# Optimization experiments

Hardware: AMD Instinct MI355X
Metric: run time of the kernel (lower is better)

Reference implementation:

```python
import jax, jax.numpy as jnp
import numpy as np

B, S = 2048, 4096
RANK = 8            # bilinear rank and gain projector rank
LOW_GAIN = 1.0
LOW_SIGMA = 0.2
HIGH_GAIN = 0.5
HIGH_CUTOFF = 0.6


def setup_inputs() -> dict:
    key = jax.random.key(0)
    ks = jax.random.split(key, 12)
    sc = 0.05
    inp = {
        "x": jax.random.normal(ks[0], (B, S), dtype=jnp.float32),
        # ComplexLinear U, V: (rank, state_size) real+imag weights
        "Ur": jax.random.normal(ks[1], (RANK, S), dtype=jnp.float32) * sc,
        "Ui": jax.random.normal(ks[2], (RANK, S), dtype=jnp.float32) * sc,
        "Vr": jax.random.normal(ks[3], (RANK, S), dtype=jnp.float32) * sc,
        "Vi": jax.random.normal(ks[4], (RANK, S), dtype=jnp.float32) * sc,
        # ComplexLinear W: (state_size, rank) -- zero-init in source; random here to exercise math
        "Wr": jax.random.normal(ks[5], (S, RANK), dtype=jnp.float32) * sc,
        "Wi": jax.random.normal(ks[6], (S, RANK), dtype=jnp.float32) * sc,
        # dynamic spectral gain MLP: Linear(2S, r) -> ReLU -> Linear(r, S)
        "P1w": jax.random.normal(ks[7], (RANK, 2 * S), dtype=jnp.float32) * 0.01,
        "P1b": jnp.zeros((RANK,), dtype=jnp.float32),
        "P2w": jax.random.normal(ks[8], (S, RANK), dtype=jnp.float32) * 0.01,
        "P2b": jax.random.normal(ks[9], (S,), dtype=jnp.float32) * 0.01,
        "alpha": jnp.ones((), dtype=jnp.float32),
    }
    return inp


def _complex_linear(z, wr, wi):
    # y = z @ (wr + i*wi)^T for complex z, real weights of shape (out, in)
    w = (wr + 1j * wi).astype(jnp.complex64)
    return z @ w.T


def _fixed_spectral_gain(nf):
    low_boost = LOW_GAIN * jnp.exp(-0.5 * jnp.square(nf / LOW_SIGMA))
    tw = max(0.05, 0.25 * max(0.05, 1.0 - HIGH_CUTOFF))
    high_damp = HIGH_GAIN * jax.nn.sigmoid((nf - HIGH_CUTOFF) / tw)
    return jnp.maximum(1.0 + low_boost - high_damp, 0.0)


def reference(x, Ur, Ui, Vr, Vi, Wr, Wi, P1w, P1b, P2w, P2b, alpha):
    s = x.shape[-1]
    z = jnp.fft.fft(x, axis=-1).astype(jnp.complex64)  # [B, S] complex spectrum

    # normalized frequency in [0, 1]
    nf = (jnp.abs(jnp.fft.fftfreq(s)) * 2.0).astype(jnp.float32)  # [S]
    base_gain = _fixed_spectral_gain(nf)                          # [S]

    # dynamic spectral delta: small MLP on concatenated real/imag spectrum features
    feat = jnp.concatenate([z.real, z.imag], axis=-1)             # [B, 2S]
    hidden = jax.nn.relu(feat @ P1w.T + P1b)                      # [B, r]
    delta = hidden @ P2w.T + P2b                                  # [B, S]

    # radial (isotropic) interpolation of delta onto the frequency grid
    pos = jnp.clip(nf, 0.0, 1.0)
    scaled = pos * (s - 1)
    lower = jnp.floor(scaled).astype(jnp.int32)
    upper = jnp.ceil(scaled).astype(jnp.int32)
    frac = (scaled - lower.astype(jnp.float32))[None, :]          # [1, S]
    d_lo = delta[:, lower]                                        # [B, S]
    d_hi = delta[:, upper]
    delta_i = d_lo + (d_hi - d_lo) * frac

    gain = jnp.maximum(base_gain[None, :] + alpha * delta_i, 0.0)  # [B, S]
    z = z * gain.astype(jnp.complex64)

    # cross-dimensional complex bilinear coupling (low rank)
    p = _complex_linear(z, Ur, Ui)          # [B, r]
    q = _complex_linear(z, Vr, Vi)          # [B, r]
    gamma = p * jnp.conj(q)                 # [B, r]
    z = z + _complex_linear(gamma, Wr, Wi)  # [B, S]

    return jnp.fft.ifft(z, axis=-1).real.astype(jnp.float32)
```

## Files before the change

### kernel.cpp

```cpp
#include <hip/hip_runtime.h>

#define S_LEN 4096
#define NT 512
#define PER 8
#define RANK 8
#define BP 4160
#define NHALF 2049
#define TWO_PI 6.2831853071795864769f

__device__ __forceinline__ void cmul(float& xr, float& xi, float cr, float ci){
    float tr = xr*cr - xi*ci;
    xi = xr*ci + xi*cr;
    xr = tr;
}

template<int SIGN>
__device__ __forceinline__ void dft4(float& ar,float& ai,float& br,float& bi,
                                     float& cr,float& ci,float& dr,float& di){
    float Ar=ar+cr, Ai=ai+ci;
    float Br=ar-cr, Bi=ai-ci;
    float Cr=br+dr, Ci=bi+di;
    float Dr, Di;
    if (SIGN < 0){ Dr = bi-di; Di = dr-br; }
    else         { Dr = di-bi; Di = br-dr; }
    ar=Ar+Cr; ai=Ai+Ci;
    br=Br+Dr; bi=Bi+Di;
    cr=Ar-Cr; ci=Ai-Ci;
    dr=Br-Dr; di=Bi-Di;
}

template<int SIGN>
__device__ __forceinline__ void dft8(float ur[8], float ui[8]){
    const float h = 0.70710678118654752f;
    float er0=ur[0], ei0=ui[0], er1=ur[2], ei1=ui[2];
    float er2=ur[4], ei2=ui[4], er3=ur[6], ei3=ui[6];
    float fr0=ur[1], fi0=ui[1], fr1=ur[3], fi1=ui[3];
    float fr2=ur[5], fi2=ui[5], fr3=ur[7], fi3=ui[7];
    dft4<SIGN>(er0,ei0, er1,ei1, er2,ei2, er3,ei3);
    dft4<SIGN>(fr0,fi0, fr1,fi1, fr2,fi2, fr3,fi3);
    {   const float c =  h, s_ = (SIGN<0) ? -h : h;
        cmul(fr1, fi1, c, s_); }
    {   float tr = fr2, ti = fi2;
        if (SIGN < 0){ fr2 =  ti; fi2 = -tr; }
        else         { fr2 = -ti; fi2 =  tr; }
    }
    {   const float c = -h, s_ = (SIGN<0) ? -h : h;
        cmul(fr3, fi3, c, s_); }
    ur[0]=er0+fr0; ui[0]=ei0+fi0;
    ur[1]=er1+fr1; ui[1]=ei1+fi1;
    ur[2]=er2+fr2; ui[2]=ei2+fi2;
    ur[3]=er3+fr3; ui[3]=ei3+fi3;
    ur[4]=er0-fr0; ui[4]=ei0-fi0;
    ur[5]=er1-fr1; ui[5]=ei1-fi1;
    ur[6]=er2-fr2; ui[6]=ei2-fi2;
    ur[7]=er3-fr3; ui[7]=ei3-fi3;
}

template<int SIGN>
__device__ __forceinline__ void twiddle8(float ur[8], float ui[8], float theta){
    float s, c;
    __sincosf(theta, &s, &c);
    const float wi = (SIGN < 0) ? -s : s;
    const float wr = c;
    float pr = wr, pi = wi;
    cmul(ur[1], ui[1], pr, pi);
#pragma unroll
    for (int m=2;m<8;m++){
        float nr = pr*wr - pi*wi;
        pi = pr*wi + pi*wr;
        pr = nr;
        cmul(ur[m], ui[m], pr, pi);
    }
}

__device__ __forceinline__ void gain_pair(int k, const float* hhA, const float* hhB,
    float alpha, const float* __restrict__ P2w, const float* __restrict__ P2b,
    float& ga, float& gb){
    float nf = (float)k * (1.0f/2048.0f);
    float tt = nf * 5.0f;
    float lb = __expf(-0.5f * tt * tt);
    float hd = 0.5f / (1.0f + __expf(-(nf - 0.6f) * 10.0f));
    float bg = fmaxf(1.0f + lb - hd, 0.0f);
    float scaled = nf * 4095.0f;
    float fl = floorf(scaled);
    int lo = (int)fl;
    int hi = (int)ceilf(scaled);
    float fr = scaled - fl;
    const float4* p2lo = (const float4*)(P2w + (size_t)lo * RANK);
    const float4* p2hi = (const float4*)(P2w + (size_t)hi * RANK);
    float4 a0 = p2lo[0], a1 = p2lo[1];
    float4 b0 = p2hi[0], b1 = p2hi[1];
    float blo = P2b[lo], bhi = P2b[hi];
    float dAlo = blo + hhA[0]*a0.x + hhA[1]*a0.y + hhA[2]*a0.z + hhA[3]*a0.w
                     + hhA[4]*a1.x + hhA[5]*a1.y + hhA[6]*a1.z + hhA[7]*a1.w;
    float dAhi = bhi + hhA[0]*b0.x + hhA[1]*b0.y + hhA[2]*b0.z + hhA[3]*b0.w
                     + hhA[4]*b1.x + hhA[5]*b1.y + hhA[6]*b1.z + hhA[7]*b1.w;
    float dBlo = blo + hhB[0]*a0.x + hhB[1]*a0.y + hhB[2]*a0.z + hhB[3]*a0.w
                     + hhB[4]*a1.x + hhB[5]*a1.y + hhB[6]*a1.z + hhB[7]*a1.w;
    float dBhi = bhi + hhB[0]*b0.x + hhB[1]*b0.y + hhB[2]*b0.z + hhB[3]*b0.w
                     + hhB[4]*b1.x + hhB[5]*b1.y + hhB[6]*b1.z + hhB[7]*b1.w;
    float dA = dAlo + (dAhi - dAlo) * fr;
    float dB = dBlo + (dBhi - dBlo) * fr;
    ga = fmaxf(bg + alpha * dA, 0.0f);
    gb = fmaxf(bg + alpha * dB, 0.0f);
}


__global__ __launch_bounds__(NT, 4) void recip_mixer(
    const float* __restrict__ x,
    const float* __restrict__ Ur, const float* __restrict__ Ui,
    const float* __restrict__ Vr, const float* __restrict__ Vi,
    const float* __restrict__ Wr, const float* __restrict__ Wi,
    const float* __restrict__ P1w, const float* __restrict__ P1b,
    const float* __restrict__ P2w, const float* __restrict__ P2b,
    const float* __restrict__ alphap,
    float* __restrict__ out)
{
    __shared__ float sre[BP], sim[BP];
    __shared__ float gA[NHALF], gB[NHALF];
    __shared__ float red[256];
    __shared__ float hidA[RANK], hidB[RANK];
    __shared__ float4 gam4[RANK];
    __shared__ float pqs[64];

    const int t    = threadIdx.x;
    const int pairidx = blockIdx.x;
    const int lane = t & 63;
    const int wid  = t >> 6;

    float ur[8], ui[8];

    const int baseA = (t & 63) + 512 * (t >> 6);
    const int baseB = (t & 7) + 8*(t >> 6) + 520*((t >> 3) & 7);
    const int baseC = (t >> 3) + 520*(t & 7);

    const float* xa = x + (size_t)(2 * pairidx) * S_LEN;
    const float* xb = xa + S_LEN;

    {
#pragma unroll
        for (int c=0;c<8;c++){ ur[c] = xa[t + 512*c]; ui[c] = xb[t + 512*c]; }
        dft8<-1>(ur, ui);
#pragma unroll
        for (int e=0;e<8;e++){ sre[baseA + 64*e] = ur[e]; sim[baseA + 64*e] = ui[e]; }
    }
    __syncthreads();
    {
#pragma unroll
        for (int m=0;m<8;m++){ ur[m] = sre[t + 512*m]; ui[m] = sim[t + 512*m]; }
        twiddle8<-1>(ur, ui, TWO_PI * (float)(t >> 6) * (1.0f/64.0f));
        dft8<-1>(ur, ui);
        __syncthreads();
#pragma unroll
        for (int e=0;e<8;e++){ sre[baseB + 64*e] = ur[e]; sim[baseB + 64*e] = ui[e]; }
    }
    __syncthreads();
    {
#pragma unroll
        for (int m=0;m<8;m++){ ur[m] = sre[t + 520*m]; ui[m] = sim[t + 520*m]; }
        twiddle8<-1>(ur, ui, TWO_PI * (float)(t >> 3) * (1.0f/512.0f));
        dft8<-1>(ur, ui);
        __syncthreads();
#pragma unroll
        for (int e=0;e<8;e++){ sre[baseC + 64*e] = ur[e]; sim[baseC + 64*e] = ui[e]; }
    }
    __syncthreads();
    {
#pragma unroll
        for (int m=0;m<8;m++){ ur[m] = sre[t + 520*m]; ui[m] = sim[t + 520*m]; }
        twiddle8<-1>(ur, ui, TWO_PI * (float)t * (1.0f/4096.0f));
        dft8<-1>(ur, ui);
        __syncthreads();
#pragma unroll
        for (int e=0;e<8;e++){ sre[t + 512*e] = ur[e]; sim[t + 512*e] = ui[e]; }
    }
    __syncthreads();

    {
        float ha[RANK], hb[RANK];
#pragma unroll
        for (int r = 0; r < RANK; r++){ ha[r] = 0.0f; hb[r] = 0.0f; }
#pragma unroll 1
        for (int i = 0; i < PER; i++) {
            int k = t + NT * i;
            int j = (S_LEN - k) & (S_LEN - 1);
            float ar = sre[k], ai = sim[k];
            float br = sre[j], bi = sim[j];
            float zar = 0.5f*(ar + br), zai = 0.5f*(ai - bi);
            float zbr = 0.5f*(ai + bi), zbi = 0.5f*(br - ar);
#pragma unroll
            for (int r = 0; r < RANK; r++) {
                float p0 = P1w[r * (2 * S_LEN) + k];
                float p1 = P1w[r * (2 * S_LEN) + S_LEN + k];
                ha[r] += zar * p0 + zai * p1;
                hb[r] += zbr * p0 + zbi * p1;
            }
        }
#pragma unroll
        for (int r = 0; r < RANK; r++) {
#pragma unroll
            for (int off = 32; off > 0; off >>= 1){
                ha[r] += __shfl_xor(ha[r], off, 64);
                hb[r] += __shfl_xor(hb[r], off, 64);
            }
        }
        if (lane == 0) {
#pragma unroll
            for (int r = 0; r < RANK; r++){
                red[wid * 16 + r]     = ha[r];
                red[wid * 16 + 8 + r] = hb[r];
            }
        }
        __syncthreads();
        if (t < 16) {
            float v = 0.0f;
#pragma unroll
            for (int w = 0; w < 8; w++) v += red[w * 16 + t];
            float res = fmaxf(v + P1b[t & 7], 0.0f);
            if (t < 8) hidA[t] = res; else hidB[t - 8] = res;
        }
        __syncthreads();
    }

    {
        float hhA[RANK], hhB[RANK];
#pragma unroll
        for (int r = 0; r < RANK; r++){ hhA[r] = hidA[r]; hhB[r] = hidB[r]; }
        const float alpha = alphap[0];
#pragma unroll 1
        for (int i = 0; i < 4; i++) {
            int k = t + 512 * i;
            float ga, gb;
            gain_pair(k, hhA, hhB, alpha, P2w, P2b, ga, gb);
            gA[k] = ga; gB[k] = gb;
        }
        if (t == 0) {
            float ga, gb;
            gain_pair(2048, hhA, hhB, alpha, P2w, P2b, ga, gb);
            gA[2048] = ga; gB[2048] = gb;
        }
    }
    __syncthreads();

    {
        float pAr[RANK], pAi[RANK], pBr[RANK], pBi[RANK];
#pragma unroll
        for (int r = 0; r < RANK; r++){ pAr[r]=0.f; pAi[r]=0.f; pBr[r]=0.f; pBi[r]=0.f; }
#pragma unroll 1
        for (int i = 0; i < PER; i++) {
            int k = t + NT * i;
            int j = (S_LEN - k) & (S_LEN - 1);
            int m = (k <= 2048) ? k : (S_LEN - k);
            float ar = sre[k], ai = sim[k];
            float br = sre[j], bi = sim[j];
            float ga = gA[m], gb = gB[m];
            float zar = 0.5f*ga*(ar + br), zai = 0.5f*ga*(ai - bi);
            float zbr = 0.5f*gb*(ai + bi), zbi = 0.5f*gb*(br - ar);
#pragma unroll
            for (int r = 0; r < RANK; r++) {
                float u_ = Ur[r * S_LEN + k], v_ = Ui[r * S_LEN + k];
                pAr[r] += zar * u_ - zai * v_;
                pAi[r] += zar * v_ + zai * u_;
                pBr[r] += zbr * u_ - zbi * v_;
                pBi[r] += zbr * v_ + zbi * u_;
            }
        }
#pragma unroll
        for (int r = 0; r < RANK; r++) {
#pragma unroll
            for (int off = 32; off > 0; off >>= 1) {
                pAr[r] += __shfl_xor(pAr[r], off, 64);
                pAi[r] += __shfl_xor(pAi[r], off, 64);
                pBr[r] += __shfl_xor(pBr[r], off, 64);
                pBi[r] += __shfl_xor(pBi[r], off, 64);
            }
        }
        if (lane == 0) {
#pragma unroll
            for (int r = 0; r < RANK; r++) {
                red[wid * 32 + r]      = pAr[r];
                red[wid * 32 + 8 + r]  = pAi[r];
                red[wid * 32 + 16 + r] = pBr[r];
                red[wid * 32 + 24 + r] = pBi[r];
            }
        }
        __syncthreads();
        if (t < 32) {
            float v = 0.0f;
#pragma unroll
            for (int w = 0; w < 8; w++) v += red[w * 32 + t];
            pqs[t] = v;
        }
        __syncthreads();
    }

    {
        float qAr[RANK], qAi[RANK], qBr[RANK], qBi[RANK];
#pragma unroll
        for (int r = 0; r < RANK; r++){ qAr[r]=0.f; qAi[r]=0.f; qBr[r]=0.f; qBi[r]=0.f; }
#pragma unroll 1
        for (int i = 0; i < PER; i++) {
            int k = t + NT * i;
            int j = (S_LEN - k) & (S_LEN - 1);
            int m = (k <= 2048) ? k : (S_LEN - k);
            float ar = sre[k], ai = sim[k];
            float br = sre[j], bi = sim[j];
            float ga = gA[m], gb = gB[m];
            float zar = 0.5f*ga*(ar + br), zai = 0.5f*ga*(ai - bi);
            float zbr = 0.5f*gb*(ai + bi), zbi = 0.5f*gb*(br - ar);
#pragma unroll
            for (int r = 0; r < RANK; r++) {
                float w_ = Vr[r * S_LEN + k], y_ = Vi[r * S_LEN + k];
                qAr[r] += zar * w_ - zai * y_;
                qAi[r] += zar * y_ + zai * w_;
                qBr[r] += zbr * w_ - zbi * y_;
                qBi[r] += zbr * y_ + zbi * w_;
            }
        }
#pragma unroll
        for (int r = 0; r < RANK; r++) {
#pragma unroll
            for (int off = 32; off > 0; off >>= 1) {
                qAr[r] += __shfl_xor(qAr[r], off, 64);
                qAi[r] += __shfl_xor(qAi[r], off, 64);
                qBr[r] += __shfl_xor(qBr[r], off, 64);
                qBi[r] += __shfl_xor(qBi[r], off, 64);
            }
        }
        if (lane == 0) {
#pragma unroll
            for (int r = 0; r < RANK; r++) {
                red[wid * 32 + r]      = qAr[r];
                red[wid * 32 + 8 + r]  = qAi[r];
                red[wid * 32 + 16 + r] = qBr[r];
                red[wid * 32 + 24 + r] = qBi[r];
            }
        }
        __syncthreads();
        if (t < 32) {
            float v = 0.0f;
#pragma unroll
            for (int w = 0; w < 8; w++) v += red[w * 32 + t];
            pqs[32 + t] = v;
        }
        __syncthreads();
        if (t < 8) {
            float paR = pqs[t],      paI = pqs[8 + t];
            float pbR = pqs[16 + t], pbI = pqs[24 + t];
            float qaR = pqs[32 + t], qaI = pqs[40 + t];
            float qbR = pqs[48 + t], qbI = pqs[56 + t];
            gam4[t] = make_float4(
                paR * qaR + paI * qaI,
                paI * qaR - paR * qaI,
                pbR * qbR + pbI * qbI,
                pbI * qbR - pbR * qbI);
        }
        __syncthreads();
    }

    {
        auto do_pair = [&](int k){
            int j = (S_LEN - k) & (S_LEN - 1);
            float ar = sre[k], ai = sim[k];
            float br = sre[j], bi = sim[j];
            float ga = gA[k], gb = gB[k];
            float zar = 0.5f*ga*(ar + br), zai = 0.5f*ga*(ai - bi);
            float zbr = 0.5f*gb*(ai + bi), zbi = 0.5f*gb*(br - ar);

            float uakr=0.f, uaki=0.f, ubkr=0.f, ubki=0.f;
            {
                const float4* WRk = (const float4*)(Wr + (size_t)k * RANK);
                const float4* WIk = (const float4*)(Wi + (size_t)k * RANK);
#pragma unroll
                for (int h2 = 0; h2 < 2; ++h2){
                    float4 w4 = WRk[h2], y4 = WIk[h2];
                    float4 g0 = gam4[4*h2+0];
                    uakr += g0.x*w4.x - g0.y*y4.x;  uaki += g0.x*y4.x + g0.y*w4.x;
                    ubkr += g0.z*w4.x - g0.w*y4.x;  ubki += g0.z*y4.x + g0.w*w4.x;
                    float4 g1 = gam4[4*h2+1];
                    uakr += g1.x*w4.y - g1.y*y4.y;  uaki += g1.x*y4.y + g1.y*w4.y;
                    ubkr += g1.z*w4.y - g1.w*y4.y;  ubki += g1.z*y4.y + g1.w*w4.y;
                    float4 g2 = gam4[4*h2+2];
                    uakr += g2.x*w4.z - g2.y*y4.z;  uaki += g2.x*y4.z + g2.y*w4.z;
                    ubkr += g2.z*w4.z - g2.w*y4.z;  ubki += g2.z*y4.z + g2.w*w4.z;
                    float4 g3 = gam4[4*h2+3];
                    uakr += g3.x*w4.w - g3.y*y4.w;  uaki += g3.x*y4.w + g3.y*w4.w;
                    ubkr += g3.z*w4.w - g3.w*y4.w;  ubki += g3.z*y4.w + g3.w*w4.w;
                }
            }
            float uajr=0.f, uaji=0.f, ubjr=0.f, ubji=0.f;
            {
                const float4* WRj = (const float4*)(Wr + (size_t)j * RANK);
                const float4* WIj = (const float4*)(Wi + (size_t)j * RANK);
#pragma unroll
                for (int h2 = 0; h2 < 2; ++h2){
                    float4 w4 = WRj[h2], y4 = WIj[h2];
                    float4 g0 = gam4[4*h2+0];
                    uajr += g0.x*w4.x - g0.y*y4.x;  uaji += g0.x*y4.x + g0.y*w4.x;
                    ubjr += g0.z*w4.x - g0.w*y4.x;  ubji += g0.z*y4.x + g0.w*w4.x;
                    float4 g1 = gam4[4*h2+1];
                    uajr += g1.x*w4.y - g1.y*y4.y;  uaji += g1.x*y4.y + g1.y*w4.y;
                    ubjr += g1.z*w4.y - g1.w*y4.y;  ubji += g1.z*y4.y + g1.w*w4.y;
                    float4 g2 = gam4[4*h2+2];
                    uajr += g2.x*w4.z - g2.y*y4.z;  uaji += g2.x*y4.z + g2.y*w4.z;
                    ubjr += g2.z*w4.z - g2.w*y4.z;  ubji += g2.z*y4.z + g2.w*w4.z;
                    float4 g3 = gam4[4*h2+3];
                    uajr += g3.x*w4.w - g3.y*y4.w;  uaji += g3.x*y4.w + g3.y*w4.w;
                    ubjr += g3.z*w4.w - g3.w*y4.w;  ubji += g3.z*y4.w + g3.w*w4.w;
                }
            }
            float HaR = zar + 0.5f*(uakr + uajr);
            float HaI = zai + 0.5f*(uaki - uaji);
            float HbR = zbr + 0.5f*(ubkr + ubjr);
            float HbI = zbi + 0.5f*(ubki - ubji);
            sre[k] = HaR - HbI;  sim[k] = HaI + HbR;
            sre[j] = HaR + HbI;  sim[j] = HbR - HaI;
        };
#pragma unroll 1
        for (int i = 0; i < 4; i++) do_pair(t + 512 * i);
        if (t == 0) do_pair(2048);
    }
    __syncthreads();

    {
#pragma unroll
        for (int c=0;c<8;c++){ ur[c] = sre[t + 512*c]; ui[c] = sim[t + 512*c]; }
        dft8<1>(ur, ui);
        __syncthreads();
#pragma unroll
        for (int e=0;e<8;e++){ sre[baseA + 64*e] = ur[e]; sim[baseA + 64*e] = ui[e]; }
    }
    __syncthreads();
    {
#pragma unroll
        for (int m=0;m<8;m++){ ur[m] = sre[t + 512*m]; ui[m] = sim[t + 512*m]; }
        twiddle8<1>(ur, ui, TWO_PI * (float)(t >> 6) * (1.0f/64.0f));
        dft8<1>(ur, ui);
        __syncthreads();
#pragma unroll
        for (int e=0;e<8;e++){ sre[baseB + 64*e] = ur[e]; sim[baseB + 64*e] = ui[e]; }
    }
    __syncthreads();
    {
#pragma unroll
        for (int m=0;m<8;m++){ ur[m] = sre[t + 520*m]; ui[m] = sim[t + 520*m]; }
        twiddle8<1>(ur, ui, TWO_PI * (float)(t >> 3) * (1.0f/512.0f));
        dft8<1>(ur, ui);
        __syncthreads();
#pragma unroll
        for (int e=0;e<8;e++){ sre[baseC + 64*e] = ur[e]; sim[baseC + 64*e] = ui[e]; }
    }
    __syncthreads();
    {
#pragma unroll
        for (int m=0;m<8;m++){ ur[m] = sre[t + 520*m]; ui[m] = sim[t + 520*m]; }
        twiddle8<1>(ur, ui, TWO_PI * (float)t * (1.0f/4096.0f));
        dft8<1>(ur, ui);
        float* orow_a = out + (size_t)(2 * pairidx) * S_LEN;
        float* orow_b = orow_a + S_LEN;
        const float scale = 1.0f / (float)S_LEN;
#pragma unroll
        for (int e=0;e<8;e++){
            orow_a[t + 512*e] = ur[e] * scale;
            orow_b[t + 512*e] = ui[e] * scale;
        }
    }
}

extern "C" void kernel_launch(void* const* d_in, const int* in_sizes, int n_in,
                              void* d_out, int out_size, void* d_ws, size_t ws_size,
                              hipStream_t stream) {
    const float* x    = (const float*)d_in[0];
    const float* Ur   = (const float*)d_in[1];
    const float* Ui   = (const float*)d_in[2];
    const float* Vr   = (const float*)d_in[3];
    const float* Vi   = (const float*)d_in[4];
    const float* Wr   = (const float*)d_in[5];
    const float* Wi   = (const float*)d_in[6];
    const float* P1w  = (const float*)d_in[7];
    const float* P1b  = (const float*)d_in[8];
    const float* P2w  = (const float*)d_in[9];
    const float* P2b  = (const float*)d_in[10];
    const float* alph = (const float*)d_in[11];

    recip_mixer<<<dim3(1024), dim3(NT), 0, stream>>>(
        x, Ur, Ui, Vr, Vi, Wr, Wi, P1w, P1b, P2w, P2b, alph, (float*)d_out);
}
```

Measured before the change: 193.4 us.

## Exploit Hermitian symmetry to halve spectral reduction loops and parallelize twiddles

The P1, U and V projection loops now walk only frequencies 0..2047. Each iteration folds the weights at k and its mirror 4096-k into combined sum and difference terms, and thread 0 handles the Nyquist bin separately. This halves the shared-memory spectrum reads and the loop trip count. Twiddle powers are now built with a shallow squaring tree instead of a serial multiply chain, which shortens the dependency chain at the cost of slightly different rounding. One barrier after the gain computation is dropped; this relies on each thread reading only the gain entries it wrote itself.

```diff
diff --git a/kernel.cpp b/kernel.cpp
--- a/kernel.cpp
+++ b/kernel.cpp
@@ -60,17 +60,21 @@
 __device__ __forceinline__ void twiddle8(float ur[8], float ui[8], float theta){
     float s, c;
     __sincosf(theta, &s, &c);
-    const float wi = (SIGN < 0) ? -s : s;
-    const float wr = c;
-    float pr = wr, pi = wi;
-    cmul(ur[1], ui[1], pr, pi);
-#pragma unroll
-    for (int m=2;m<8;m++){
-        float nr = pr*wr - pi*wi;
-        pi = pr*wi + pi*wr;
-        pr = nr;
-        cmul(ur[m], ui[m], pr, pi);
-    }
+    const float w1i = (SIGN < 0) ? -s : s;
+    const float w1r = c;
+    float w2r = w1r*w1r - w1i*w1i, w2i = 2.0f*w1r*w1i;
+    float w3r = w2r*w1r - w2i*w1i, w3i = w2r*w1i + w2i*w1r;
+    float w4r = w2r*w2r - w2i*w2i, w4i = 2.0f*w2r*w2i;
+    float w5r = w4r*w1r - w4i*w1i, w5i = w4r*w1i + w4i*w1r;
+    float w6r = w3r*w3r - w3i*w3i, w6i = 2.0f*w3r*w3i;
+    float w7r = w4r*w3r - w4i*w3i, w7i = w4r*w3i + w4i*w3r;
+    cmul(ur[1], ui[1], w1r, w1i);
+    cmul(ur[2], ui[2], w2r, w2i);
+    cmul(ur[3], ui[3], w3r, w3i);
+    cmul(ur[4], ui[4], w4r, w4i);
+    cmul(ur[5], ui[5], w5r, w5i);
+    cmul(ur[6], ui[6], w6r, w6i);
+    cmul(ur[7], ui[7], w7r, w7i);
 }
 
 __device__ __forceinline__ void gain_pair(int k, const float* hhA, const float* hhB,
@@ -181,19 +185,32 @@
 #pragma unroll
         for (int r = 0; r < RANK; r++){ ha[r] = 0.0f; hb[r] = 0.0f; }
 #pragma unroll 1
-        for (int i = 0; i < PER; i++) {
-            int k = t + NT * i;
+        for (int i = 0; i < 4; i++) {
+            int k = t + 512 * i;
             int j = (S_LEN - k) & (S_LEN - 1);
+            float jm = (k == 0) ? 0.0f : 1.0f;
             float ar = sre[k], ai = sim[k];
             float br = sre[j], bi = sim[j];
             float zar = 0.5f*(ar + br), zai = 0.5f*(ai - bi);
             float zbr = 0.5f*(ai + bi), zbi = 0.5f*(br - ar);
 #pragma unroll
             for (int r = 0; r < RANK; r++) {
-                float p0 = P1w[r * (2 * S_LEN) + k];
-                float p1 = P1w[r * (2 * S_LEN) + S_LEN + k];
-                ha[r] += zar * p0 + zai * p1;
-                hb[r] += zbr * p0 + zbi * p1;
+                const float* P1r = P1w + r * (2 * S_LEN);
+                float p0k = P1r[k],        p1k = P1r[S_LEN + k];
+                float p0j = P1r[j],        p1j = P1r[S_LEN + j];
+                float us = fmaf(jm, p0j, p0k);
+                float ud = fmaf(-jm, p1j, p1k);
+                ha[r] += zar * us + zai * ud;
+                hb[r] += zbr * us + zbi * ud;
+            }
+        }
+        if (t == 0) {
+            float ar = sre[2048], ai = sim[2048];
+#pragma unroll
+            for (int r = 0; r < RANK; r++) {
+                float p0 = P1w[r * (2 * S_LEN) + 2048];
+                ha[r] += ar * p0;
+                hb[r] += ai * p0;
             }
         }
 #pragma unroll
@@ -240,29 +257,46 @@
             gA[2048] = ga; gB[2048] = gb;
         }
     }
-    __syncthreads();
 
     {
         float pAr[RANK], pAi[RANK], pBr[RANK], pBi[RANK];
 #pragma unroll
         for (int r = 0; r < RANK; r++){ pAr[r]=0.f; pAi[r]=0.f; pBr[r]=0.f; pBi[r]=0.f; }
 #pragma unroll 1
-        for (int i = 0; i < PER; i++) {
-            int k = t + NT * i;
+        for (int i = 0; i < 4; i++) {
+            int k = t + 512 * i;
             int j = (S_LEN - k) & (S_LEN - 1);
-            int m = (k <= 2048) ? k : (S_LEN - k);
+            float jm = (k == 0) ? 0.0f : 1.0f;
             float ar = sre[k], ai = sim[k];
             float br = sre[j], bi = sim[j];
-            float ga = gA[m], gb = gB[m];
+            float ga = gA[k], gb = gB[k];
             float zar = 0.5f*ga*(ar + br), zai = 0.5f*ga*(ai - bi);
             float zbr = 0.5f*gb*(ai + bi), zbi = 0.5f*gb*(br - ar);
 #pragma unroll
             for (int r = 0; r < RANK; r++) {
-                float u_ = Ur[r * S_LEN + k], v_ = Ui[r * S_LEN + k];
-                pAr[r] += zar * u_ - zai * v_;
-                pAi[r] += zar * v_ + zai * u_;
-                pBr[r] += zbr * u_ - zbi * v_;
-                pBi[r] += zbr * v_ + zbi * u_;
+                const float* Urr = Ur + r * S_LEN;
+                const float* Uir = Ui + r * S_LEN;
+                float ukr = Urr[k], uki = Uir[k];
+                float ujr = Urr[j], uji = Uir[j];
+                float us = fmaf(jm, ujr, ukr);
+                float ud = fmaf(-jm, ujr, ukr);
+                float vs = fmaf(jm, uji, uki);
+                float vd = fmaf(-jm, uji, uki);
+                pAr[r] += zar * us - zai * vd;
+                pAi[r] += zar * vs + zai * ud;
+                pBr[r] += zbr * us - zbi * vd;
+                pBi[r] += zbr * vs + zbi * ud;
+            }
+        }
+        if (t == 0) {
+            float ar = sre[2048], ai = sim[2048];
+            float zar = gA[2048] * ar;
+            float zbr = gB[2048] * ai;
+#pragma unroll
+            for (int r = 0; r < RANK; r++) {
+                float ukr = Ur[r * S_LEN + 2048], uki = Ui[r * S_LEN + 2048];
+                pAr[r] += zar * ukr;  pAi[r] += zar * uki;
+                pBr[r] += zbr * ukr;  pBi[r] += zbr * uki;
             }
         }
 #pragma unroll
@@ -299,22 +333,40 @@
 #pragma unroll
         for (int r = 0; r < RANK; r++){ qAr[r]=0.f; qAi[r]=0.f; qBr[r]=0.f; qBi[r]=0.f; }
 #pragma unroll 1
-        for (int i = 0; i < PER; i++) {
-            int k = t + NT * i;
+        for (int i = 0; i < 4; i++) {
+            int k = t + 512 * i;
             int j = (S_LEN - k) & (S_LEN - 1);
-            int m = (k <= 2048) ? k : (S_LEN - k);
+            float jm = (k == 0) ? 0.0f : 1.0f;
             float ar = sre[k], ai = sim[k];
             float br = sre[j], bi = sim[j];
-            float ga = gA[m], gb = gB[m];
+            float ga = gA[k], gb = gB[k];
             float zar = 0.5f*ga*(ar + br), zai = 0.5f*ga*(ai - bi);
             float zbr = 0.5f*gb*(ai + bi), zbi = 0.5f*gb*(br - ar);
 #pragma unroll
             for (int r = 0; r < RANK; r++) {
-                float w_ = Vr[r * S_LEN + k], y_ = Vi[r * S_LEN + k];
-                qAr[r] += zar * w_ - zai * y_;
-                qAi[r] += zar * y_ + zai * w_;
-                qBr[r] += zbr * w_ - zbi * y_;
-                qBi[r] += zbr * y_ + zbi * w_;
+                const float* Vrr = Vr + r * S_LEN;
+                const float* Vir = Vi + r * S_LEN;
+                float wkr = Vrr[k], wki = Vir[k];
+                float wjr = Vrr[j], wji = Vir[j];
+                float us = fmaf(jm, wjr, wkr);
+                float ud = fmaf(-jm, wjr, wkr);
+                float vs = fmaf(jm, wji, wki);
+                float vd = fmaf(-jm, wji, wki);
+                qAr[r] += zar * us - zai * vd;
+                qAi[r] += zar * vs + zai * ud;
+                qBr[r] += zbr * us - zbi * vd;
+                qBi[r] += zbr * vs + zbi * ud;
+            }
+        }
+        if (t == 0) {
+            float ar = sre[2048], ai = sim[2048];
+            float zar = gA[2048] * ar;
+            float zbr = gB[2048] * ai;
+#pragma unroll
+            for (int r = 0; r < RANK; r++) {
+                float wkr = Vr[r * S_LEN + 2048], wki = Vi[r * S_LEN + 2048];
+                qAr[r] += zar * wkr;  qAi[r] += zar * wki;
+                qBr[r] += zbr * wkr;  qBi[r] += zbr * wki;
             }
         }
 #pragma unroll
```

Result: faster. 184.9 us (-4.4%).
